# Optimization experiments

Measured on AMD Instinct MI355X. Metric: run time of the kernel, lower is better.

Reference implementation:

```python
import jax, jax.numpy as jnp
import numpy as np

jax.config.update("jax_enable_x64", True)

# config
B, S = 4, 4096
H_SIZE = 2048          # hidden_size
VOCAB = 128000         # engram_base_vocab_size
MAX_NGRAM = 3          # engram_max_ngram_size -> orders 2..3
PRIME = 500009         # engram_n_embed_per_ngram (same prime for every order)
N_HEAD = 4             # engram_n_head_per_ngram
E = 32                 # engram_embed_dim
KS = 4                 # short conv kernel size
NUM_ORDERS = MAX_NGRAM - 1
TOTAL_HEADS = NUM_ORDERS * N_HEAD
TOTAL_ROWS = PRIME * N_HEAD * NUM_ORDERS  # flat multi-head table rows


def setup_inputs() -> dict:
    key = jax.random.key(0)
    k_ids, k_h, k_tab, k_cw, k_hp, k_gp, k_op = jax.random.split(key, 7)
    input_ids = jax.random.randint(k_ids, (B, S), 0, VOCAB, dtype=jnp.int64)
    hidden_states = jax.random.normal(k_h, (B, S, H_SIZE), dtype=jnp.float32)
    # identity compressed-tokenizer mapping buffer
    mapping = jnp.arange(VOCAB, dtype=jnp.int64)
    # deterministic odd multipliers, seeded like _build_multipliers
    rng = np.random.default_rng(0 * 10007 + 0 * 1009)
    mults = rng.integers(1, 2 ** 31, size=(NUM_ORDERS, N_HEAD, MAX_NGRAM))
    multipliers = jnp.asarray(mults * 2 + 1, dtype=jnp.int64)
    table = 0.02 * jax.random.normal(k_tab, (TOTAL_ROWS, E), dtype=jnp.float32)
    conv_w = 0.1 * jax.random.normal(k_cw, (E, KS), dtype=jnp.float32)  # depthwise taps
    conv_b = jnp.zeros((E,), dtype=jnp.float32)
    Wh = 0.05 * jax.random.normal(k_hp, (E, TOTAL_HEADS * E), dtype=jnp.float32)
    Wg = 0.02 * jax.random.normal(k_gp, (E, H_SIZE), dtype=jnp.float32)
    Wo = 0.02 * jax.random.normal(k_op, (H_SIZE, E), dtype=jnp.float32)
    return {"input_ids": input_ids, "hidden_states": hidden_states,
            "mapping": mapping, "multipliers": multipliers, "table": table,
            "conv_w": conv_w, "conv_b": conv_b, "Wh": Wh, "Wg": Wg, "Wo": Wo}


def _hash_indices(compressed, multipliers):
    """XOR-mix n-gram hash indices -> [B, S, TOTAL_HEADS] int64."""
    all_idx = []
    offset = 0
    for oi, k in enumerate(range(2, MAX_NGRAM + 1)):
        # forward sliding window, clamped at last token (matches cat/expand trick)
        pos = jnp.minimum(jnp.arange(S)[:, None] + jnp.arange(k)[None, :], S - 1)  # [S,k]
        ng = compressed[:, pos]                                  # [B,S,k]
        m = multipliers[oi, :, :k]                               # [nh,k]
        prod = ng[:, :, None, :] * m[None, None, :, :]           # [B,S,nh,k]
        h = prod[..., 0]
        for p in range(1, k):
            h = h ^ prod[..., p]
        idx = h % PRIME + (offset + jnp.arange(N_HEAD, dtype=jnp.int64) * PRIME)
        all_idx.append(idx)
        offset += PRIME * N_HEAD
    return jnp.concatenate(all_idx, axis=-1)


def reference(input_ids, hidden_states, mapping, multipliers, table,
              conv_w, conv_b, Wh, Wg, Wo):
    compressed = mapping[input_ids]                              # [B,S]
    indices = _hash_indices(compressed, multipliers)             # [B,S,TOTAL_HEADS]
    emb = table[indices].reshape(B, S, TOTAL_HEADS * E)          # multi-head gather
    emb = emb @ Wh.T                                             # head_proj -> [B,S,E]
    # causal depthwise short conv (kernel KS, left pad KS-1)
    xp = jnp.pad(emb, ((0, 0), (KS - 1, 0), (0, 0)))
    emb = sum(xp[:, j:j + S, :] * conv_w[:, j] for j in range(KS)) + conv_b
    gate = jax.nn.sigmoid(hidden_states @ Wg.T)                  # [B,S,E]
    return (gate * emb) @ Wo.T                                   # [B,S,H_SIZE]
```

## Files before the change

### kernel.cpp

```cpp
#include <hip/hip_runtime.h>
#include <hip/hip_bf16.h>
#include <stdint.h>

#define HSZ 2048
#define PRIME 500009u
#define CHUNK 64
#define NCH 32

typedef __attribute__((ext_vector_type(8))) short short8;
typedef __attribute__((ext_vector_type(4))) float f32x4;
typedef __attribute__((ext_vector_type(4))) unsigned uint4v;
typedef __attribute__((ext_vector_type(2))) unsigned uint2v;

#define MEMFENCE asm volatile("" ::: "memory")
#define BARRIER() do { MEMFENCE; __builtin_amdgcn_s_barrier(); MEMFENCE; } while (0)
#define WAIT_LGKM0 asm volatile("s_waitcnt lgkmcnt(0)" ::: "memory")
#define WAIT_VM(n) asm volatile("s_waitcnt vmcnt(" #n ")" ::: "memory")

__device__ __forceinline__ unsigned pk2(float x, float y) {
  __hip_bfloat162 h = __float22bfloat162_rn(make_float2(x, y));
  return *reinterpret_cast<unsigned*>(&h);
}
__device__ __forceinline__ short f2bf(float f) {
  __hip_bfloat16 h = __float2bfloat16(f);
  return *reinterpret_cast<short*>(&h);
}
__device__ __forceinline__ short8 pack8(float4 a, float4 b) {
  uint4v u = {pk2(a.x, a.y), pk2(a.z, a.w), pk2(b.x, b.y), pk2(b.z, b.w)};
  return __builtin_bit_cast(short8, u);
}
__device__ __forceinline__ short8 load8_bf(const float* __restrict__ p) {
  float4 a = *reinterpret_cast<const float4*>(p);
  float4 b = *reinterpret_cast<const float4*>(p + 4);
  return pack8(a, b);
}
__device__ __forceinline__ void gload_lds16(const float* g, void* l) {
  __builtin_amdgcn_global_load_lds(
      (const __attribute__((address_space(1))) void*)g,
      (__attribute__((address_space(3))) void*)l, 16, 0, 0);
}

__global__ __launch_bounds__(256, 2) void engram_fused(
    const int* __restrict__ ids, const int* __restrict__ mapping,
    const unsigned* __restrict__ mult, const float* __restrict__ table,
    const float* __restrict__ Wh, const float* __restrict__ hidden,
    const float* __restrict__ cw, const float* __restrict__ cb,
    const float* __restrict__ Wg, const float* __restrict__ Wo,
    float* __restrict__ out) {
  __shared__ __align__(16) float hbuf[2][32][CHUNK];
  __shared__ __align__(16) float wgbuf[2][32][CHUNK];
  __shared__ __align__(16) short A_lds[48][264];
  __shared__ __align__(16) float emb48[48][36];
  __shared__ float emb_c[32][33];
  __shared__ __align__(16) short ge_lds[32][40];
  __shared__ int idx_lds[384];

  const int tid = threadIdx.x;
  const int wid = tid >> 6, lane = tid & 63;
  const int l16 = lane & 15, q = lane >> 4;
  const int t0 = blockIdx.x * 32;

  auto STAGE = [&](int buf, int kc) {
#pragma unroll
    for (int j = 0; j < 2; ++j) {
      int r0 = wid * 8 + j * 4;
      int r = r0 + (lane >> 4);
      unsigned c4 = (((unsigned)l16 * 16u) ^ (((unsigned)r & 7u) << 4)) >> 2;
      const float* src = hidden + (size_t)(t0 + r) * HSZ + kc * CHUNK + c4;
      gload_lds16(src, &hbuf[buf][r0][0]);
    }
#pragma unroll
    for (int j = 0; j < 2; ++j) {
      int r0 = wid * 8 + j * 4;
      int r = r0 + (lane >> 4);
      unsigned c4 = (((unsigned)l16 * 16u) ^ (((unsigned)r & 7u) << 4)) >> 2;
      const float* src = Wg + (size_t)r * HSZ + kc * CHUNK + c4;
      gload_lds16(src, &wgbuf[buf][r0][0]);
    }
  };

  STAGE(0, 0);
  STAGE(1, 1);

#pragma unroll
  for (int p = 0; p < 2; ++p) {
    int hh = p * 256 + tid;
    if (hh < 384) {
      int slot = hh >> 3, head = hh & 7;
      int tg = t0 - 16 + slot;
      if (tg < 0) tg = 0;
      int b = tg >> 12, s = tg & 4095;
      const int* idb = ids + (b << 12);
      int s1 = s + 1 > 4095 ? 4095 : s + 1;
      int s2 = s + 2 > 4095 ? 4095 : s + 2;
      uint64_t c0 = (unsigned)mapping[idb[s]];
      uint64_t c1 = (unsigned)mapping[idb[s1]];
      uint64_t c2 = (unsigned)mapping[idb[s2]];
      int mb = head * 3;
      uint64_t h = (c0 * (uint64_t)mult[mb]) ^ (c1 * (uint64_t)mult[mb + 1]);
      if (head >= 4) h ^= c2 * (uint64_t)mult[mb + 2];
      idx_lds[hh] = (int)((unsigned)(h % PRIME) + (unsigned)head * PRIME);
    }
  }
  WAIT_LGKM0; BARRIER();

#pragma unroll
  for (int p = 0; p < 12; ++p) {
    int r = p * 32 + (tid >> 3);
    int c4 = (tid & 7) * 4;
    int row = idx_lds[r];
    float4 v = *reinterpret_cast<const float4*>(table + (size_t)row * 32 + c4);
    uint2v pk = {pk2(v.x, v.y), pk2(v.z, v.w)};
    *reinterpret_cast<uint2v*>(&A_lds[r >> 3][(r & 7) * 32 + c4]) = pk;
  }
  WAIT_LGKM0; BARRIER();

  for (int job = wid; job < 6; job += 4) {
    int jt = job >> 1, e0 = (job & 1) * 16;
    f32x4 acc = {0.f, 0.f, 0.f, 0.f};
#pragma unroll
    for (int ks = 0; ks < 8; ++ks) {
      short8 wf = load8_bf(Wh + (size_t)(e0 + l16) * 256 + ks * 32 + q * 8);
      short8 a = *reinterpret_cast<const short8*>(&A_lds[jt * 16 + l16][ks * 32 + q * 8]);
      acc = __builtin_amdgcn_mfma_f32_16x16x32_bf16(wf, a, acc, 0, 0, 0);
    }
    *reinterpret_cast<f32x4*>(&emb48[jt * 16 + l16][e0 + q * 4]) = acc;
  }
  WAIT_LGKM0; BARRIER();

#pragma unroll
  for (int it = 0; it < 4; ++it) {
    int ii = it * 256 + tid;
    int tl = ii >> 5, e = ii & 31;
    int s = (t0 & 4095) + tl;
    float a = cb[e];
#pragma unroll
    for (int j = 0; j < 4; ++j)
      if (s - 3 + j >= 0) a += cw[e * 4 + j] * emb48[13 + tl + j][e];
    emb_c[tl][e] = a;
  }
  WAIT_LGKM0; BARRIER();

  const int tt = wid >> 1, ee = wid & 1;
  const int R = tt * 16 + l16;
  const unsigned sw = ((unsigned)R & 7u) << 4;
  const char* hb0 = (const char*)&hbuf[0][R][0];
  const char* hb1 = (const char*)&hbuf[1][R][0];
  const int Rb = ee * 16 + l16;
  const unsigned swb = ((unsigned)Rb & 7u) << 4;
  const char* wb0 = (const char*)&wgbuf[0][Rb][0];
  const char* wb1 = (const char*)&wgbuf[1][Rb][0];
  f32x4 acc = {0.f, 0.f, 0.f, 0.f};

  for (int kc = 0; kc < NCH - 1; ++kc) {
    WAIT_VM(4);
    BARRIER();
    const char* hb = (kc & 1) ? hb1 : hb0;
    const char* wb = (kc & 1) ? wb1 : wb0;
    unsigned x0 = q * 32u;
    float4 a0 = *reinterpret_cast<const float4*>(hb + (x0 ^ sw));
    float4 a1 = *reinterpret_cast<const float4*>(hb + ((x0 + 16) ^ sw));
    float4 a2 = *reinterpret_cast<const float4*>(hb + ((x0 + 128) ^ sw));
    float4 a3 = *reinterpret_cast<const float4*>(hb + ((x0 + 144) ^ sw));
    float4 b0 = *reinterpret_cast<const float4*>(wb + (x0 ^ swb));
    float4 b1 = *reinterpret_cast<const float4*>(wb + ((x0 + 16) ^ swb));
    float4 b2 = *reinterpret_cast<const float4*>(wb + ((x0 + 128) ^ swb));
    float4 b3 = *reinterpret_cast<const float4*>(wb + ((x0 + 144) ^ swb));
    short8 A0 = pack8(a0, a1), A1 = pack8(a2, a3);
    short8 B0 = pack8(b0, b1), B1 = pack8(b2, b3);
    WAIT_LGKM0;
    BARRIER();
    if (kc < NCH - 2) STAGE(kc & 1, kc + 2);
    acc = __builtin_amdgcn_mfma_f32_16x16x32_bf16(A0, B0, acc, 0, 0, 0);
    acc = __builtin_amdgcn_mfma_f32_16x16x32_bf16(A1, B1, acc, 0, 0, 0);
  }
  {
    WAIT_VM(0);
    BARRIER();
    unsigned x0 = q * 32u;
    float4 a0 = *reinterpret_cast<const float4*>(hb1 + (x0 ^ sw));
    float4 a1 = *reinterpret_cast<const float4*>(hb1 + ((x0 + 16) ^ sw));
    float4 a2 = *reinterpret_cast<const float4*>(hb1 + ((x0 + 128) ^ sw));
    float4 a3 = *reinterpret_cast<const float4*>(hb1 + ((x0 + 144) ^ sw));
    float4 b0 = *reinterpret_cast<const float4*>(wb1 + (x0 ^ swb));
    float4 b1 = *reinterpret_cast<const float4*>(wb1 + ((x0 + 16) ^ swb));
    float4 b2 = *reinterpret_cast<const float4*>(wb1 + ((x0 + 128) ^ swb));
    float4 b3 = *reinterpret_cast<const float4*>(wb1 + ((x0 + 144) ^ swb));
    acc = __builtin_amdgcn_mfma_f32_16x16x32_bf16(pack8(a0, a1), pack8(b0, b1), acc, 0, 0, 0);
    acc = __builtin_amdgcn_mfma_f32_16x16x32_bf16(pack8(a2, a3), pack8(b2, b3), acc, 0, 0, 0);
  }

#pragma unroll
  for (int j = 0; j < 4; ++j) {
    int r = tt * 16 + q * 4 + j, c = ee * 16 + l16;
    float g = 1.f / (1.f + __expf(-acc[j]));
    ge_lds[r][c] = f2bf(g * emb_c[r][c]);
  }
  WAIT_LGKM0; BARRIER();

  short8 Af0 = *reinterpret_cast<const short8*>(&ge_lds[l16][q * 8]);
  short8 Af1 = *reinterpret_cast<const short8*>(&ge_lds[16 + l16][q * 8]);
  float* orow0 = out + (size_t)(t0 + l16) * HSZ;
  float* orow1 = out + (size_t)(t0 + 16 + l16) * HSZ;
  int hbase = wid * 512;
  for (int ht = 0; ht < 32; ++ht) {
    int h0 = hbase + ht * 16;
    short8 aw = load8_bf(Wo + (size_t)(h0 + l16) * 32 + q * 8);
    f32x4 z = {0.f, 0.f, 0.f, 0.f};
    f32x4 o0 = __builtin_amdgcn_mfma_f32_16x16x32_bf16(aw, Af0, z, 0, 0, 0);
    f32x4 o1 = __builtin_amdgcn_mfma_f32_16x16x32_bf16(aw, Af1, z, 0, 0, 0);
    *reinterpret_cast<f32x4*>(orow0 + h0 + q * 4) = o0;
    *reinterpret_cast<f32x4*>(orow1 + h0 + q * 4) = o1;
  }
}

extern "C" void kernel_launch(void* const* d_in, const int* in_sizes, int n_in,
                              void* d_out, int out_size, void* d_ws, size_t ws_size,
                              hipStream_t stream) {
  const int* ids = (const int*)d_in[0];
  const float* hidden = (const float*)d_in[1];
  const int* mapping = (const int*)d_in[2];
  const unsigned* mult = (const unsigned*)d_in[3];
  const float* table = (const float*)d_in[4];
  const float* cw = (const float*)d_in[5];
  const float* cb = (const float*)d_in[6];
  const float* Wh = (const float*)d_in[7];
  const float* Wg = (const float*)d_in[8];
  const float* Wo = (const float*)d_in[9];
  float* out = (float*)d_out;

  engram_fused<<<512, 256, 0, stream>>>(ids, mapping, mult, table, Wh, hidden,
                                        cw, cb, Wg, Wo, out);
}
```

Measured before the change: 76.91 us.

## Shrink halo rows and overlap table gather with gate GEMM loop

The causal conv halo drops from 16 to 4 preceding tokens, so only 36 token slots are hashed and gathered instead of 48. The table gather is now issued into registers before the hidden/Wg staging starts, so its latency hides behind the gate GEMM pipeline. The head projection and conv run after that loop, with the third MFMA tile overlapping the second (base row 20, partial store). This holds 9 float4 values in registers across the main loop, which raises register pressure, and the vmcnt wait in the loop is adjusted to account for the extra outstanding loads.

```diff
diff --git a/kernel.cpp b/kernel.cpp
--- a/kernel.cpp
+++ b/kernel.cpp
@@ -49,11 +49,11 @@
     float* __restrict__ out) {
   __shared__ __align__(16) float hbuf[2][32][CHUNK];
   __shared__ __align__(16) float wgbuf[2][32][CHUNK];
-  __shared__ __align__(16) short A_lds[48][264];
-  __shared__ __align__(16) float emb48[48][36];
+  __shared__ __align__(16) short A_lds[36][264];
+  __shared__ __align__(16) float emb36[36][36];
   __shared__ float emb_c[32][33];
   __shared__ __align__(16) short ge_lds[32][40];
-  __shared__ int idx_lds[384];
+  __shared__ int idx_lds[288];
 
   const int tid = threadIdx.x;
   const int wid = tid >> 6, lane = tid & 63;
@@ -66,28 +66,24 @@
       int r0 = wid * 8 + j * 4;
       int r = r0 + (lane >> 4);
       unsigned c4 = (((unsigned)l16 * 16u) ^ (((unsigned)r & 7u) << 4)) >> 2;
-      const float* src = hidden + (size_t)(t0 + r) * HSZ + kc * CHUNK + c4;
-      gload_lds16(src, &hbuf[buf][r0][0]);
+      gload_lds16(hidden + (size_t)(t0 + r) * HSZ + kc * CHUNK + c4,
+                  &hbuf[buf][r0][0]);
     }
 #pragma unroll
     for (int j = 0; j < 2; ++j) {
       int r0 = wid * 8 + j * 4;
       int r = r0 + (lane >> 4);
       unsigned c4 = (((unsigned)l16 * 16u) ^ (((unsigned)r & 7u) << 4)) >> 2;
-      const float* src = Wg + (size_t)r * HSZ + kc * CHUNK + c4;
-      gload_lds16(src, &wgbuf[buf][r0][0]);
+      gload_lds16(Wg + (size_t)r * HSZ + kc * CHUNK + c4, &wgbuf[buf][r0][0]);
     }
   };
-
-  STAGE(0, 0);
-  STAGE(1, 1);
 
 #pragma unroll
   for (int p = 0; p < 2; ++p) {
     int hh = p * 256 + tid;
-    if (hh < 384) {
+    if (hh < 288) {
       int slot = hh >> 3, head = hh & 7;
-      int tg = t0 - 16 + slot;
+      int tg = t0 - 4 + slot;
       if (tg < 0) tg = 0;
       int b = tg >> 12, s = tg & 4095;
       const int* idb = ids + (b << 12);
@@ -104,42 +100,17 @@
   }
   WAIT_LGKM0; BARRIER();
 
-#pragma unroll
-  for (int p = 0; p < 12; ++p) {
-    int r = p * 32 + (tid >> 3);
-    int c4 = (tid & 7) * 4;
+  float4 g[9];
+#pragma unroll
+  for (int p = 0; p < 9; ++p) {
+    int task = p * 256 + tid;
+    int r = task >> 3, c4 = (task & 7) * 4;
     int row = idx_lds[r];
-    float4 v = *reinterpret_cast<const float4*>(table + (size_t)row * 32 + c4);
-    uint2v pk = {pk2(v.x, v.y), pk2(v.z, v.w)};
-    *reinterpret_cast<uint2v*>(&A_lds[r >> 3][(r & 7) * 32 + c4]) = pk;
-  }
-  WAIT_LGKM0; BARRIER();
-
-  for (int job = wid; job < 6; job += 4) {
-    int jt = job >> 1, e0 = (job & 1) * 16;
-    f32x4 acc = {0.f, 0.f, 0.f, 0.f};
-#pragma unroll
-    for (int ks = 0; ks < 8; ++ks) {
-      short8 wf = load8_bf(Wh + (size_t)(e0 + l16) * 256 + ks * 32 + q * 8);
-      short8 a = *reinterpret_cast<const short8*>(&A_lds[jt * 16 + l16][ks * 32 + q * 8]);
-      acc = __builtin_amdgcn_mfma_f32_16x16x32_bf16(wf, a, acc, 0, 0, 0);
-    }
-    *reinterpret_cast<f32x4*>(&emb48[jt * 16 + l16][e0 + q * 4]) = acc;
-  }
-  WAIT_LGKM0; BARRIER();
-
-#pragma unroll
-  for (int it = 0; it < 4; ++it) {
-    int ii = it * 256 + tid;
-    int tl = ii >> 5, e = ii & 31;
-    int s = (t0 & 4095) + tl;
-    float a = cb[e];
-#pragma unroll
-    for (int j = 0; j < 4; ++j)
-      if (s - 3 + j >= 0) a += cw[e * 4 + j] * emb48[13 + tl + j][e];
-    emb_c[tl][e] = a;
-  }
-  WAIT_LGKM0; BARRIER();
+    g[p] = *reinterpret_cast<const float4*>(table + (size_t)row * 32 + c4);
+  }
+
+  STAGE(0, 0);
+  STAGE(1, 1);
 
   const int tt = wid >> 1, ee = wid & 1;
   const int R = tt * 16 + l16;
@@ -153,7 +124,7 @@
   f32x4 acc = {0.f, 0.f, 0.f, 0.f};
 
   for (int kc = 0; kc < NCH - 1; ++kc) {
-    WAIT_VM(4);
+    WAIT_VM(3);
     BARRIER();
     const char* hb = (kc & 1) ? hb1 : hb0;
     const char* wb = (kc & 1) ? wb1 : wb0;
@@ -191,10 +162,48 @@
   }
 
 #pragma unroll
+  for (int p = 0; p < 9; ++p) {
+    int task = p * 256 + tid;
+    int r = task >> 3, c4 = (task & 7) * 4;
+    uint2v pk = {pk2(g[p].x, g[p].y), pk2(g[p].z, g[p].w)};
+    *reinterpret_cast<uint2v*>(&A_lds[r >> 3][(r & 7) * 32 + c4]) = pk;
+  }
+  WAIT_LGKM0; BARRIER();
+
+  for (int job = wid; job < 6; job += 4) {
+    int jt = job >> 1;
+    int base = (jt == 0) ? 0 : (jt == 1) ? 16 : 20;
+    int e0 = (job & 1) * 16;
+    f32x4 ac = {0.f, 0.f, 0.f, 0.f};
+#pragma unroll
+    for (int ks = 0; ks < 8; ++ks) {
+      short8 wf = load8_bf(Wh + (size_t)(e0 + l16) * 256 + ks * 32 + q * 8);
+      short8 a = *reinterpret_cast<const short8*>(&A_lds[base + l16][ks * 32 + q * 8]);
+      ac = __builtin_amdgcn_mfma_f32_16x16x32_bf16(wf, a, ac, 0, 0, 0);
+    }
+    if (jt != 2 || l16 >= 12)
+      *reinterpret_cast<f32x4*>(&emb36[base + l16][e0 + q * 4]) = ac;
+  }
+  WAIT_LGKM0; BARRIER();
+
+#pragma unroll
+  for (int it = 0; it < 4; ++it) {
+    int ii = it * 256 + tid;
+    int tl = ii >> 5, e = ii & 31;
+    int s = (t0 & 4095) + tl;
+    float a = cb[e];
+#pragma unroll
+    for (int j = 0; j < 4; ++j)
+      if (s - 3 + j >= 0) a += cw[e * 4 + j] * emb36[tl + 1 + j][e];
+    emb_c[tl][e] = a;
+  }
+  WAIT_LGKM0; BARRIER();
+
+#pragma unroll
   for (int j = 0; j < 4; ++j) {
     int r = tt * 16 + q * 4 + j, c = ee * 16 + l16;
-    float g = 1.f / (1.f + __expf(-acc[j]));
-    ge_lds[r][c] = f2bf(g * emb_c[r][c]);
+    float gt = 1.f / (1.f + __expf(-acc[j]));
+    ge_lds[r][c] = f2bf(gt * emb_c[r][c]);
   }
   WAIT_LGKM0; BARRIER();
 
```

Result: faster. 75.39 us (-2.0%).
